# Performance work log

Measured on AMD Instinct MI355X. Metric: run time of the kernel, lower is better.

The kernel has to match this reference:

```python
import jax, jax.numpy as jnp
import numpy as np

BATCH, SEQ, H_IN, N_STATE, H_OUT = 16, 4096, 128, 256, 128
RMIN, RMAX, MAX_PHASE = 0.9, 1.0, 6.283


def setup_inputs() -> dict:
    key = jax.random.key(0)
    ks = jax.random.split(key, 9)
    u = jax.random.normal(ks[0], (BATCH, SEQ, H_IN), jnp.float32)
    # LRU exponential parameterization init (matches torch __init__)
    u1 = jax.random.uniform(ks[1], (N_STATE,), jnp.float32)
    u2 = jax.random.uniform(ks[2], (N_STATE,), jnp.float32)
    nu_log = jnp.log(-0.5 * jnp.log(u1 * (RMAX + RMIN) * (RMAX - RMIN) + RMIN ** 2))
    theta_log = jnp.log(MAX_PHASE * u2)
    lam_abs = jnp.exp(-jnp.exp(nu_log))
    gamma_log = jnp.log(jnp.sqrt(1.0 - lam_abs ** 2))
    s2in = np.sqrt(2.0 * H_IN).astype(np.float32)
    B_re = jax.random.normal(ks[3], (N_STATE, H_IN), jnp.float32) / s2in
    B_im = jax.random.normal(ks[4], (N_STATE, H_IN), jnp.float32) / s2in
    sst = np.sqrt(float(N_STATE)).astype(np.float32)
    C_re = jax.random.normal(ks[5], (H_OUT, N_STATE), jnp.float32) / sst
    C_im = jax.random.normal(ks[6], (H_OUT, N_STATE), jnp.float32) / sst
    D = jax.random.normal(ks[7], (H_OUT, H_IN), jnp.float32) / np.sqrt(float(H_IN)).astype(np.float32)
    return dict(u=u, nu_log=nu_log, theta_log=theta_log, gamma_log=gamma_log,
                B_re=B_re, B_im=B_im, C_re=C_re, C_im=C_im, D=D)


def _combine(a, b):
    # complex affine composition: (l, x) o (l', x') -> (l*l', l'*x + x')
    l1r, l1i, x1r, x1i = a
    l2r, l2i, x2r, x2i = b
    lr = l1r * l2r - l1i * l2i
    li = l1r * l2i + l1i * l2r
    xr = l2r * x1r - l2i * x1i + x2r
    xi = l2r * x1i + l2i * x1r + x2i
    return (lr, li, xr, xi)


def reference(u, nu_log, theta_log, gamma_log, B_re, B_im, C_re, C_im, D):
    lam_mod = jnp.exp(-jnp.exp(nu_log))          # |lambda|, [N]
    th = jnp.exp(theta_log)
    lam_re = lam_mod * jnp.cos(th)
    lam_im = lam_mod * jnp.sin(th)
    gammas = jnp.exp(gamma_log)                  # [N]
    # input projection Bu_t = gamma * (B @ u_t), complex -> real/imag parts
    Bu_re = jnp.einsum('blh,nh->bln', u, B_re) * gammas  # [B,L,N]
    Bu_im = jnp.einsum('blh,nh->bln', u, B_im) * gammas
    Bsz, L, N = Bu_re.shape
    lr = jnp.broadcast_to(lam_re, (Bsz, L, N))
    li = jnp.broadcast_to(lam_im, (Bsz, L, N))
    # parallel scan of x_t = lambda * x_{t-1} + Bu_t, x0 = 0
    _, _, xr, xi = jax.lax.associative_scan(_combine, (lr, li, Bu_re, Bu_im), axis=1)
    zero = jnp.zeros((Bsz, 1, N), u.dtype)
    pre_re = jnp.concatenate([zero, xr[:, :-1]], axis=1)  # states[:, :-1]
    pre_im = jnp.concatenate([zero, xi[:, :-1]], axis=1)
    # y_t = Re(C x_{t-1}) + D u_t
    y = (jnp.einsum('bln,on->blo', pre_re, C_re)
         - jnp.einsum('bln,on->blo', pre_im, C_im)
         + jnp.einsum('blh,oh->blo', u, D))
    return y
```

## Files before the change

### kernel.cpp

```cpp
#include <hip/hip_runtime.h>
#include <math.h>

#define BATCH 16
#define SEQ   4096
#define HIN   128
#define NST   256
#define HOUT  128
#define CL    32
#define NC    (SEQ/CL)
#define ROWS  (BATCH*SEQ)
#define KTOT  640
#define NPRE  512

typedef __attribute__((ext_vector_type(8))) short short8;
typedef __attribute__((ext_vector_type(4))) float f32x4;

__device__ inline unsigned short f2bf(float f) {
  union { float f; unsigned u; } v; v.f = f;
  unsigned r = v.u + 0x7FFFu + ((v.u >> 16) & 1u);
  return (unsigned short)(r >> 16);
}
__device__ inline float bf2f(unsigned short s) {
  union { unsigned u; float f; } v; v.u = ((unsigned)s) << 16;
  return v.f;
}
__device__ inline float bits2f(unsigned u) {
  union { unsigned u; float f; } v; v.u = u; return v.f;
}

__global__ __launch_bounds__(256) void k_prep(
    const float* __restrict__ nu_log, const float* __restrict__ theta_log,
    const float* __restrict__ gamma_log,
    const float* __restrict__ Bre, const float* __restrict__ Bim,
    const float* __restrict__ Cre, const float* __restrict__ Cim,
    const float* __restrict__ Dm,
    float* __restrict__ lamre, float* __restrict__ lamim,
    unsigned* __restrict__ lamPk,
    unsigned short* __restrict__ Wb, unsigned short* __restrict__ W) {
  int idx = blockIdx.x*256 + threadIdx.x;
  if (idx < NST) {
    float lm = expf(-expf(nu_log[idx]));
    float th = expf(theta_log[idx]);
    float lr = lm * cosf(th), li = lm * sinf(th);
    lamre[idx] = lr; lamim[idx] = li;
    float pr = 1.f, pi = 0.f;
    for (int j = 0; j < CL; ++j) {
      lamPk[j*NST + idx] = ((unsigned)f2bf(pi) << 16) | (unsigned)f2bf(pr);
      float nr = pr*lr - pi*li;
      float ni = pr*li + pi*lr;
      pr = nr; pi = ni;
    }
  }
  if (idx < 512*HIN) {
    int r = idx >> 7, h = idx & 127;
    int g = r >> 7;
    int w = r & 127;
    int n = g*64 + (w & 63);
    float gm = expf(gamma_log[n]);
    float v = (w < 64) ? Bre[n*HIN + h] : Bim[n*HIN + h];
    Wb[idx] = f2bf(gm * v);
  }
  if (idx < HOUT*KTOT) {
    int o = idx / KTOT, k = idx - o*KTOT;
    float v;
    if (k < NST)        v =  Cre[o*NST + k];
    else if (k < 2*NST) v = -Cim[o*NST + (k - NST)];
    else                v =  Dm[o*HIN + (k - 2*NST)];
    W[idx] = f2bf(v);
  }
}

union SharedBu {
  unsigned short B[128][136];
  float stg[2][32][132];
};
__global__ __launch_bounds__(256) void k_bu(
    const float* __restrict__ u, const unsigned short* __restrict__ Wb,
    const float* __restrict__ lamre, const float* __restrict__ lamim,
    unsigned short* __restrict__ preL,
    float* __restrict__ S_re, float* __restrict__ S_im) {
  __shared__ unsigned short Asl[128][136];
  __shared__ SharedBu sh;
  int tid = threadIdx.x;
  int row0 = blockIdx.x * 128;
  int wid = tid >> 6, lane = tid & 63;
  int lm = lane & 15, lq = lane >> 4;
  int m0 = (wid >> 1) * 64, n0 = (wid & 1) * 64;
  int b = row0 >> 12;
  int cbase = (row0 & 4095) >> 5;
#pragma unroll
  for (int cc = 0; cc < 8; ++cc) {
    int ch = cc*256 + tid;
    int r = ch >> 4, h0 = (ch & 15) * 8;
    const float* src = u + (size_t)(row0 + r)*HIN + h0;
    float4 v0 = *(const float4*)src;
    float4 v1 = *(const float4*)(src + 4);
    unsigned short o[8];
    o[0]=f2bf(v0.x); o[1]=f2bf(v0.y); o[2]=f2bf(v0.z); o[3]=f2bf(v0.w);
    o[4]=f2bf(v1.x); o[5]=f2bf(v1.y); o[6]=f2bf(v1.z); o[7]=f2bf(v1.w);
    *(short8*)&Asl[r][h0] = *(const short8*)o;
  }
  for (int g = 0; g < 4; ++g) {
    __syncthreads();
#pragma unroll
    for (int cc = 0; cc < 8; ++cc) {
      int ch = cc*256 + tid;
      int r = ch >> 4, h0 = (ch & 15) * 8;
      *(short8*)&sh.B[r][h0] = *(const short8*)&Wb[(size_t)(g*128 + r)*HIN + h0];
    }
    __syncthreads();
    f32x4 acc[4][4];
#pragma unroll
    for (int i = 0; i < 4; ++i)
#pragma unroll
      for (int j = 0; j < 4; ++j) acc[i][j] = (f32x4)0.f;
#pragma unroll
    for (int ks = 0; ks < 4; ++ks) {
      int k0 = ks*32 + lq*8;
      short8 a[4], bb[4];
#pragma unroll
      for (int i = 0; i < 4; ++i) a[i] = *(const short8*)&Asl[m0 + i*16 + lm][k0];
#pragma unroll
      for (int j = 0; j < 4; ++j) bb[j] = *(const short8*)&sh.B[n0 + j*16 + lm][k0];
#pragma unroll
      for (int i = 0; i < 4; ++i)
#pragma unroll
        for (int j = 0; j < 4; ++j)
          acc[i][j] = __builtin_amdgcn_mfma_f32_16x16x32_bf16(a[i], bb[j], acc[i][j], 0, 0, 0);
    }
    for (int p = 0; p < 2; ++p) {
      __syncthreads();
#pragma unroll
      for (int ii = 0; ii < 2; ++ii) {
        int i = 2*p + ii;
#pragma unroll
        for (int j = 0; j < 4; ++j)
#pragma unroll
          for (int r = 0; r < 4; ++r) {
            int trow = ii*16 + lq*4 + r;
            sh.stg[wid >> 1][trow][n0 + j*16 + lm] = acc[i][j][r];
          }
      }
      __syncthreads();
      if (tid < 128) {
        int buf = tid >> 6, nl = tid & 63;
        int ng = g*64 + nl;
        float lr = lamre[ng], li = lamim[ng];
        float rr[CL], ri[CL];
#pragma unroll
        for (int t = 0; t < CL; ++t) {
          rr[t] = sh.stg[buf][t][nl];
          ri[t] = sh.stg[buf][t][64 + nl];
        }
        int rowb = row0 + buf*64 + p*32;
        unsigned short* pl = preL + (size_t)rowb*NPRE;
        float sr = 0.f, si = 0.f;
#pragma unroll
        for (int t = 0; t < CL; ++t) {
          pl[ng]       = f2bf(sr);
          pl[NST + ng] = f2bf(si);
          float nr = lr*sr - li*si + rr[t];
          float ni = lr*si + li*sr + ri[t];
          sr = nr; si = ni; pl += NPRE;
        }
        int c = cbase + buf*2 + p;
        int idx = (b*NC + c)*NST + ng;
        S_re[idx] = sr; S_im[idx] = si;
      }
    }
  }
}

__global__ __launch_bounds__(256) void k_carry2(
    const float* __restrict__ S_re, const float* __restrict__ S_im,
    const float* __restrict__ lamre, const float* __restrict__ lamim,
    float* __restrict__ G_re, float* __restrict__ G_im) {
  int blk = blockIdx.x;
  int b = blk >> 3, g = blk & 7;
  int n = threadIdx.x;
  float ar = lamre[n], ai = lamim[n];
#pragma unroll
  for (int s = 0; s < 5; ++s) { float nr = ar*ar - ai*ai, ni = 2.f*ar*ai; ar = nr; ai = ni; }
  float sre[16], sim[16];
#pragma unroll
  for (int cc = 0; cc < 16; ++cc) {
    int idx = (b*NC + g*16 + cc)*NST + n;
    sre[cc] = S_re[idx]; sim[cc] = S_im[idx];
  }
  float tr = 0.f, ti = 0.f;
#pragma unroll
  for (int cc = 0; cc < 16; ++cc) {
    float nr = ar*tr - ai*ti + sre[cc];
    float ni = ar*ti + ai*tr + sim[cc];
    tr = nr; ti = ni;
  }
  int gi = (b*8 + g)*NST + n;
  G_re[gi] = tr; G_im[gi] = ti;
}

__global__ __launch_bounds__(256) void k_final(
    const float* __restrict__ S_re, const float* __restrict__ S_im,
    const float* __restrict__ G_re, const float* __restrict__ G_im,
    const float* __restrict__ lamre, const float* __restrict__ lamim,
    unsigned* __restrict__ X0Pk) {
  int blk = blockIdx.x;
  int b = blk >> 3, g = blk & 7;
  int n = threadIdx.x;
  float ar = lamre[n], ai = lamim[n];
#pragma unroll
  for (int s = 0; s < 5; ++s) { float nr = ar*ar - ai*ai, ni = 2.f*ar*ai; ar = nr; ai = ni; }
  float a5r = ar, a5i = ai;
#pragma unroll
  for (int s = 0; s < 4; ++s) { float nr = a5r*a5r - a5i*a5i, ni = 2.f*a5r*a5i; a5r = nr; a5i = ni; }
  float gr_[7], gi_[7];
#pragma unroll
  for (int j = 0; j < 7; ++j) {
    if (j < g) { int gi2 = (b*8 + j)*NST + n; gr_[j] = G_re[gi2]; gi_[j] = G_im[gi2]; }
    else       { gr_[j] = 0.f; gi_[j] = 0.f; }
  }
  float pr = 0.f, pi = 0.f;
#pragma unroll
  for (int j = 0; j < 7; ++j) {
    if (j < g) {
      float nr = a5r*pr - a5i*pi + gr_[j];
      float ni = a5r*pi + a5i*pr + gi_[j];
      pr = nr; pi = ni;
    }
  }
  float sre[16], sim[16];
#pragma unroll
  for (int cc = 0; cc < 16; ++cc) {
    int idx = (b*NC + g*16 + cc)*NST + n;
    sre[cc] = S_re[idx]; sim[cc] = S_im[idx];
  }
  float xr = pr, xi = pi;
#pragma unroll
  for (int cc = 0; cc < 16; ++cc) {
    int idx = (b*NC + g*16 + cc)*NST + n;
    X0Pk[idx] = ((unsigned)f2bf(xi) << 16) | (unsigned)f2bf(xr);
    float nr = ar*xr - ai*xi + sre[cc];
    float ni = ar*xi + ai*xr + sim[cc];
    xr = nr; xi = ni;
  }
}

__global__ __launch_bounds__(256) void k_out2(
    const unsigned short* __restrict__ preL, const float* __restrict__ u,
    const unsigned short* __restrict__ W,
    const unsigned* __restrict__ lamPk, const unsigned* __restrict__ X0Pk,
    float* __restrict__ y) {
  __shared__ unsigned short Asl[128][136];
  __shared__ unsigned short Bsl[128][136];
  int tid = threadIdx.x;
  int row0 = blockIdx.x * 128;
  int wid = tid >> 6, lane = tid & 63;
  int lm = lane & 15, lq = lane >> 4;
  int m0 = wid * 32;
  f32x4 acc[2][8];
#pragma unroll
  for (int i = 0; i < 2; ++i)
#pragma unroll
    for (int j = 0; j < 8; ++j) acc[i][j] = (f32x4)0.f;
  for (int s = 0; s < 5; ++s) {
    __syncthreads();
#pragma unroll
    for (int cc = 0; cc < 8; ++cc) {
      int ch = cc*256 + tid;
      int r = ch >> 4, h0 = (ch & 15) * 8;
      *(short8*)&Bsl[r][h0] = *(const short8*)&W[(size_t)r*KTOT + s*128 + h0];
    }
    if (s < 4) {
#pragma unroll
      for (int cc = 0; cc < 8; ++cc) {
        int ch = cc*256 + tid;
        int r = ch >> 4, h0 = (ch & 15) * 8;
        int grow = row0 + r;
        int j32 = r & 31;
        int cidx = grow >> 5;
        int n = ((s & 1) << 7) + h0;
        short8 loc = *(const short8*)&preL[(size_t)grow*NPRE + s*128 + h0];
        uint4 lp0 = *(const uint4*)&lamPk[j32*NST + n];
        uint4 lp1 = *(const uint4*)&lamPk[j32*NST + n + 4];
        uint4 xp0 = *(const uint4*)&X0Pk[(size_t)cidx*NST + n];
        uint4 xp1 = *(const uint4*)&X0Pk[(size_t)cidx*NST + n + 4];
        unsigned lps[8] = {lp0.x, lp0.y, lp0.z, lp0.w, lp1.x, lp1.y, lp1.z, lp1.w};
        unsigned xps[8] = {xp0.x, xp0.y, xp0.z, xp0.w, xp1.x, xp1.y, xp1.z, xp1.w};
        unsigned short o[8];
#pragma unroll
        for (int e = 0; e < 8; ++e) {
          float lr = bits2f(lps[e] << 16);
          float li = bits2f(lps[e] & 0xFFFF0000u);
          float xr = bits2f(xps[e] << 16);
          float xi = bits2f(xps[e] & 0xFFFF0000u);
          float lv = bf2f((unsigned short)loc[e]);
          float v = (s < 2) ? (lv + lr*xr - li*xi)
                            : (lv + lr*xi + li*xr);
          o[e] = f2bf(v);
        }
        *(short8*)&Asl[r][h0] = *(const short8*)o;
      }
    } else {
#pragma unroll
      for (int cc = 0; cc < 8; ++cc) {
        int ch = cc*256 + tid;
        int r = ch >> 4, h0 = (ch & 15) * 8;
        const float* src = u + (size_t)(row0 + r)*HIN + h0;
        float4 v0 = *(const float4*)src;
        float4 v1 = *(const float4*)(src + 4);
        unsigned short o[8];
        o[0]=f2bf(v0.x); o[1]=f2bf(v0.y); o[2]=f2bf(v0.z); o[3]=f2bf(v0.w);
        o[4]=f2bf(v1.x); o[5]=f2bf(v1.y); o[6]=f2bf(v1.z); o[7]=f2bf(v1.w);
        *(short8*)&Asl[r][h0] = *(const short8*)o;
      }
    }
    __syncthreads();
#pragma unroll
    for (int ks = 0; ks < 4; ++ks) {
      int k0 = ks*32 + lq*8;
      short8 a[2], bb[8];
#pragma unroll
      for (int i = 0; i < 2; ++i) a[i] = *(const short8*)&Asl[m0 + i*16 + lm][k0];
#pragma unroll
      for (int j = 0; j < 8; ++j) bb[j] = *(const short8*)&Bsl[j*16 + lm][k0];
#pragma unroll
      for (int i = 0; i < 2; ++i)
#pragma unroll
        for (int j = 0; j < 8; ++j)
          acc[i][j] = __builtin_amdgcn_mfma_f32_16x16x32_bf16(a[i], bb[j], acc[i][j], 0, 0, 0);
    }
  }
#pragma unroll
  for (int i = 0; i < 2; ++i)
#pragma unroll
    for (int j = 0; j < 8; ++j)
#pragma unroll
      for (int r = 0; r < 4; ++r)
        y[(size_t)(row0 + m0 + i*16 + lq*4 + r)*HOUT + j*16 + lm] = acc[i][j][r];
}

extern "C" void kernel_launch(void* const* d_in, const int* in_sizes, int n_in,
                              void* d_out, int out_size, void* d_ws, size_t ws_size,
                              hipStream_t stream) {
  const float* u         = (const float*)d_in[0];
  const float* nu_log    = (const float*)d_in[1];
  const float* theta_log = (const float*)d_in[2];
  const float* gamma_log = (const float*)d_in[3];
  const float* B_re      = (const float*)d_in[4];
  const float* B_im      = (const float*)d_in[5];
  const float* C_re      = (const float*)d_in[6];
  const float* C_im      = (const float*)d_in[7];
  const float* Dm        = (const float*)d_in[8];
  float* y = (float*)d_out;
  char* ws = (char*)d_ws;

  size_t off = 0;
  float* lamre = (float*)(ws + off);            off += 1024;
  float* lamim = (float*)(ws + off);            off += 1024;
  unsigned* lamPk = (unsigned*)(ws + off);      off += 32768;
  unsigned short* Wb = (unsigned short*)(ws + off); off += 131072;
  unsigned short* W  = (unsigned short*)(ws + off); off += 163840;
  unsigned short* preL = (unsigned short*)(ws + off); off += (size_t)ROWS*NPRE*2;
  float* S_re = (float*)(ws + off);             off += 2097152;
  float* S_im = (float*)(ws + off);             off += 2097152;
  float* G_re = (float*)(ws + off);             off += 131072;
  float* G_im = (float*)(ws + off);             off += 131072;
  unsigned* X0Pk = (unsigned*)(ws + off);       off += 2097152;

  k_prep<<<320, 256, 0, stream>>>(nu_log, theta_log, gamma_log, B_re, B_im,
                                  C_re, C_im, Dm, lamre, lamim, lamPk, Wb, W);
  k_bu<<<ROWS/128, 256, 0, stream>>>(u, Wb, lamre, lamim, preL, S_re, S_im);
  k_carry2<<<BATCH*8, 256, 0, stream>>>(S_re, S_im, lamre, lamim, G_re, G_im);
  k_final<<<BATCH*8, 256, 0, stream>>>(S_re, S_im, G_re, G_im, lamre, lamim, X0Pk);
  k_out2<<<ROWS/128, 256, 0, stream>>>(preL, u, W, lamPk, X0Pk, y);
}
```

Before: 162.9 us.

## Stage Bu tile in bf16 for single-pass chunk scan; merge carry kernels into one

```diff
diff --git a/kernel.cpp b/kernel.cpp
--- a/kernel.cpp
+++ b/kernel.cpp
@@ -72,7 +72,7 @@
 
 union SharedBu {
   unsigned short B[128][136];
-  float stg[2][32][132];
+  unsigned short stgb[4][32][132];
 };
 __global__ __launch_bounds__(256) void k_bu(
     const float* __restrict__ u, const unsigned short* __restrict__ Wb,
@@ -128,119 +128,83 @@
         for (int j = 0; j < 4; ++j)
           acc[i][j] = __builtin_amdgcn_mfma_f32_16x16x32_bf16(a[i], bb[j], acc[i][j], 0, 0, 0);
     }
-    for (int p = 0; p < 2; ++p) {
-      __syncthreads();
-#pragma unroll
-      for (int ii = 0; ii < 2; ++ii) {
-        int i = 2*p + ii;
-#pragma unroll
-        for (int j = 0; j < 4; ++j)
-#pragma unroll
-          for (int r = 0; r < 4; ++r) {
-            int trow = ii*16 + lq*4 + r;
-            sh.stg[wid >> 1][trow][n0 + j*16 + lm] = acc[i][j][r];
-          }
-      }
-      __syncthreads();
-      if (tid < 128) {
-        int buf = tid >> 6, nl = tid & 63;
-        int ng = g*64 + nl;
-        float lr = lamre[ng], li = lamim[ng];
-        float rr[CL], ri[CL];
-#pragma unroll
-        for (int t = 0; t < CL; ++t) {
-          rr[t] = sh.stg[buf][t][nl];
-          ri[t] = sh.stg[buf][t][64 + nl];
+    __syncthreads();
+#pragma unroll
+    for (int i = 0; i < 4; ++i)
+#pragma unroll
+      for (int j = 0; j < 4; ++j)
+#pragma unroll
+        for (int r = 0; r < 4; ++r) {
+          int row = m0 + i*16 + lq*4 + r;
+          sh.stgb[row >> 5][row & 31][n0 + j*16 + lm] = f2bf(acc[i][j][r]);
         }
-        int rowb = row0 + buf*64 + p*32;
-        unsigned short* pl = preL + (size_t)rowb*NPRE;
-        float sr = 0.f, si = 0.f;
-#pragma unroll
-        for (int t = 0; t < CL; ++t) {
-          pl[ng]       = f2bf(sr);
-          pl[NST + ng] = f2bf(si);
-          float nr = lr*sr - li*si + rr[t];
-          float ni = lr*si + li*sr + ri[t];
-          sr = nr; si = ni; pl += NPRE;
-        }
-        int c = cbase + buf*2 + p;
-        int idx = (b*NC + c)*NST + ng;
-        S_re[idx] = sr; S_im[idx] = si;
-      }
-    }
-  }
-}
-
-__global__ __launch_bounds__(256) void k_carry2(
+    __syncthreads();
+    {
+      int ck = tid >> 6, nl = tid & 63;
+      int ng = g*64 + nl;
+      float lr = lamre[ng], li = lamim[ng];
+      float rr[CL], ri[CL];
+#pragma unroll
+      for (int t = 0; t < CL; ++t) {
+        rr[t] = bf2f(sh.stgb[ck][t][nl]);
+        ri[t] = bf2f(sh.stgb[ck][t][64 + nl]);
+      }
+      int rowb = row0 + ck*32;
+      unsigned short* pl = preL + (size_t)rowb*NPRE;
+      float sr = 0.f, si = 0.f;
+#pragma unroll
+      for (int t = 0; t < CL; ++t) {
+        pl[ng]       = f2bf(sr);
+        pl[NST + ng] = f2bf(si);
+        float nr = lr*sr - li*si + rr[t];
+        float ni = lr*si + li*sr + ri[t];
+        sr = nr; si = ni; pl += NPRE;
+      }
+      int c = cbase + ck;
+      int idx = (b*NC + c)*NST + ng;
+      S_re[idx] = sr; S_im[idx] = si;
+    }
+  }
+}
+
+__global__ __launch_bounds__(64) void k_scan(
     const float* __restrict__ S_re, const float* __restrict__ S_im,
     const float* __restrict__ lamre, const float* __restrict__ lamim,
-    float* __restrict__ G_re, float* __restrict__ G_im) {
-  int blk = blockIdx.x;
-  int b = blk >> 3, g = blk & 7;
-  int n = threadIdx.x;
+    unsigned* __restrict__ X0Pk) {
+  int b = blockIdx.x >> 2;
+  int n = (blockIdx.x & 3) * 64 + threadIdx.x;
   float ar = lamre[n], ai = lamim[n];
 #pragma unroll
   for (int s = 0; s < 5; ++s) { float nr = ar*ar - ai*ai, ni = 2.f*ar*ai; ar = nr; ai = ni; }
-  float sre[16], sim[16];
-#pragma unroll
-  for (int cc = 0; cc < 16; ++cc) {
-    int idx = (b*NC + g*16 + cc)*NST + n;
-    sre[cc] = S_re[idx]; sim[cc] = S_im[idx];
-  }
-  float tr = 0.f, ti = 0.f;
-#pragma unroll
-  for (int cc = 0; cc < 16; ++cc) {
-    float nr = ar*tr - ai*ti + sre[cc];
-    float ni = ar*ti + ai*tr + sim[cc];
-    tr = nr; ti = ni;
-  }
-  int gi = (b*8 + g)*NST + n;
-  G_re[gi] = tr; G_im[gi] = ti;
-}
-
-__global__ __launch_bounds__(256) void k_final(
-    const float* __restrict__ S_re, const float* __restrict__ S_im,
-    const float* __restrict__ G_re, const float* __restrict__ G_im,
-    const float* __restrict__ lamre, const float* __restrict__ lamim,
-    unsigned* __restrict__ X0Pk) {
-  int blk = blockIdx.x;
-  int b = blk >> 3, g = blk & 7;
-  int n = threadIdx.x;
-  float ar = lamre[n], ai = lamim[n];
-#pragma unroll
-  for (int s = 0; s < 5; ++s) { float nr = ar*ar - ai*ai, ni = 2.f*ar*ai; ar = nr; ai = ni; }
-  float a5r = ar, a5i = ai;
-#pragma unroll
-  for (int s = 0; s < 4; ++s) { float nr = a5r*a5r - a5i*a5i, ni = 2.f*a5r*a5i; a5r = nr; a5i = ni; }
-  float gr_[7], gi_[7];
-#pragma unroll
-  for (int j = 0; j < 7; ++j) {
-    if (j < g) { int gi2 = (b*8 + j)*NST + n; gr_[j] = G_re[gi2]; gi_[j] = G_im[gi2]; }
-    else       { gr_[j] = 0.f; gi_[j] = 0.f; }
-  }
-  float pr = 0.f, pi = 0.f;
-#pragma unroll
-  for (int j = 0; j < 7; ++j) {
-    if (j < g) {
-      float nr = a5r*pr - a5i*pi + gr_[j];
-      float ni = a5r*pi + a5i*pr + gi_[j];
-      pr = nr; pi = ni;
-    }
-  }
-  float sre[16], sim[16];
-#pragma unroll
-  for (int cc = 0; cc < 16; ++cc) {
-    int idx = (b*NC + g*16 + cc)*NST + n;
-    sre[cc] = S_re[idx]; sim[cc] = S_im[idx];
-  }
-  float xr = pr, xi = pi;
-#pragma unroll
-  for (int cc = 0; cc < 16; ++cc) {
-    int idx = (b*NC + g*16 + cc)*NST + n;
-    X0Pk[idx] = ((unsigned)f2bf(xi) << 16) | (unsigned)f2bf(xr);
-    float nr = ar*xr - ai*xi + sre[cc];
-    float ni = ar*xi + ai*xr + sim[cc];
-    xr = nr; xi = ni;
+  const float* Sr = S_re + (size_t)b*NC*NST + n;
+  const float* Si = S_im + (size_t)b*NC*NST + n;
+  unsigned* Xp = X0Pk + (size_t)b*NC*NST + n;
+  float Are[16], Aim[16], Bre[16], Bim[16];
+#pragma unroll
+  for (int cc = 0; cc < 16; ++cc) { Are[cc] = Sr[cc*NST]; Aim[cc] = Si[cc*NST]; }
+  float xr = 0.f, xi = 0.f;
+#pragma unroll
+  for (int seg = 0; seg < 8; ++seg) {
+    if (seg < 7) {
+      const float* pr = Sr + (size_t)(seg+1)*16*NST;
+      const float* pi = Si + (size_t)(seg+1)*16*NST;
+      if (seg & 1) {
+#pragma unroll
+        for (int cc = 0; cc < 16; ++cc) { Are[cc] = pr[cc*NST]; Aim[cc] = pi[cc*NST]; }
+      } else {
+#pragma unroll
+        for (int cc = 0; cc < 16; ++cc) { Bre[cc] = pr[cc*NST]; Bim[cc] = pi[cc*NST]; }
+      }
+    }
+#pragma unroll
+    for (int cc = 0; cc < 16; ++cc) {
+      Xp[(size_t)(seg*16 + cc)*NST] = ((unsigned)f2bf(xi) << 16) | (unsigned)f2bf(xr);
+      float cr = (seg & 1) ? Bre[cc] : Are[cc];
+      float ci = (seg & 1) ? Bim[cc] : Aim[cc];
+      float nr = ar*xr - ai*xi + cr;
+      float ni = ar*xi + ai*xr + ci;
+      xr = nr; xi = ni;
+    }
   }
 }
 
@@ -362,14 +326,11 @@
   unsigned short* preL = (unsigned short*)(ws + off); off += (size_t)ROWS*NPRE*2;
   float* S_re = (float*)(ws + off);             off += 2097152;
   float* S_im = (float*)(ws + off);             off += 2097152;
-  float* G_re = (float*)(ws + off);             off += 131072;
-  float* G_im = (float*)(ws + off);             off += 131072;
   unsigned* X0Pk = (unsigned*)(ws + off);       off += 2097152;
 
   k_prep<<<320, 256, 0, stream>>>(nu_log, theta_log, gamma_log, B_re, B_im,
                                   C_re, C_im, Dm, lamre, lamim, lamPk, Wb, W);
   k_bu<<<ROWS/128, 256, 0, stream>>>(u, Wb, lamre, lamim, preL, S_re, S_im);
-  k_carry2<<<BATCH*8, 256, 0, stream>>>(S_re, S_im, lamre, lamim, G_re, G_im);
-  k_final<<<BATCH*8, 256, 0, stream>>>(S_re, S_im, G_re, G_im, lamre, lamim, X0Pk);
+  k_scan<<<64, 64, 0, stream>>>(S_re, S_im, lamre, lamim, X0Pk);
   k_out2<<<ROWS/128, 256, 0, stream>>>(preL, u, W, lamPk, X0Pk, y);
 }
```

Result: no change. 165.7 us (+1.7%).
